# Kernel tuning notes

Hardware: AMD Instinct MI355X
Metric: run time of the kernel (lower is better)

## Reference

```python
import jax, jax.numpy as jnp
import numpy as np

IN_DIM = 1024
OUT_DIM = 1024
L = 4
HIDDEN = 64
EMB_DIM = 2 + 2 * 2 * L  # 18
BATCH = 8192
W0 = 30.0


def make_embedded_coords():
    gy, gx = jnp.meshgrid(jnp.linspace(-1.0, 1.0, OUT_DIM), jnp.linspace(-1.0, 1.0, IN_DIM), indexing='ij')
    coords = jnp.stack([gy, gx], axis=-1).reshape(-1, 2)  # [rows*cols, 2]
    embeds = [coords]
    for i in range(L):
        freq = 2.0 ** i
        embeds.append(jnp.sin(freq * jnp.pi * coords))
        embeds.append(jnp.cos(freq * jnp.pi * coords))
    return jnp.concatenate(embeds, axis=-1)  # [rows*cols, 18]


def setup_inputs() -> dict:
    key = jax.random.key(0)
    ks = jax.random.split(key, 8)
    # init scales matching torch code
    u = lambda k, shape, b: jax.random.uniform(k, shape, jnp.float32, -b, b)
    W1 = u(ks[0], (HIDDEN, EMB_DIM), 1.0 / EMB_DIM)
    b1 = u(ks[1], (HIDDEN,), 1.0 / np.sqrt(EMB_DIM))
    s2 = np.sqrt(6.0 / HIDDEN) / W0
    W2 = u(ks[2], (HIDDEN, HIDDEN), s2)
    b2 = u(ks[3], (HIDDEN,), 1.0 / np.sqrt(HIDDEN))
    W3 = u(ks[4], (1, HIDDEN), s2)
    b3 = u(ks[5], (1,), 1.0 / np.sqrt(HIDDEN))
    x = jax.random.normal(ks[6], (BATCH, IN_DIM), jnp.float32)
    bias = jnp.zeros((OUT_DIM,), jnp.float32)
    return {
        'x': x,
        'embedded_coords': make_embedded_coords(),
        'W1': W1, 'b1': b1, 'W2': W2, 'b2': b2, 'W3': W3, 'b3': b3,
        'bias': bias,
    }


def reference(x, embedded_coords, W1, b1, W2, b2, W3, b3, bias):
    rows = bias.shape[0]
    cols = x.shape[-1]
    # tiny fully-fused hypernet MLP over rows*cols coordinate points
    h = jnp.sin(W0 * (embedded_coords @ W1.T + b1))  # [rows*cols, 64]
    h = jnp.sin(W0 * (h @ W2.T + b2))                # [rows*cols, 64]
    W = (h @ W3.T + b3).reshape(rows, cols)          # generated weight
    return x @ W.T + bias                            # [batch, out_dim]
```

## Files before the change

### kernel.cpp

```cpp
#include <hip/hip_runtime.h>
#include <hip/hip_bf16.h>


typedef __attribute__((ext_vector_type(8))) short bf16x8;
typedef __attribute__((ext_vector_type(4))) float f32x4;

#define SIN_SCALE 4.77464829275686f

__device__ __forceinline__ unsigned short f2bf(float f) {
    union { float f; unsigned u; } v; v.f = f;
    unsigned r = v.u + 0x7fffu + ((v.u >> 16) & 1u);
    return (unsigned short)(r >> 16);
}

__device__ __forceinline__ unsigned pktrunc(float a, float b) {
    union { float f; unsigned u; } x, y; x.f = a; y.f = b;
    return (x.u >> 16) | (y.u & 0xffff0000u);
}

__device__ __forceinline__ float sinrev(float x) {
    return __builtin_amdgcn_sinf(x);
}

template <int OFF>
__device__ __forceinline__ float swz_add(float v) {
    return v + __int_as_float(__builtin_amdgcn_ds_swizzle(__float_as_int(v), OFF));
}

__device__ __forceinline__ void async_ld16(const void* g, void* l) {
    __builtin_amdgcn_global_load_lds(
        (__attribute__((address_space(1))) void*)g,
        (__attribute__((address_space(3))) void*)l, 16, 0, 0);
}

__global__ __launch_bounds__(256) void prep_kernel(
        const float4* __restrict__ x, unsigned short* __restrict__ xb,
        const float* __restrict__ ec,
        const float* __restrict__ W1, const float* __restrict__ b1,
        float* __restrict__ Zrow, float* __restrict__ Zcol) {
    int b = blockIdx.x;
    if (b < 8192) {
        long i = (long)b * 256 + threadIdx.x;
        float4 v = x[i];
        ushort4 o;
        o.x = f2bf(v.x); o.y = f2bf(v.y); o.z = f2bf(v.z); o.w = f2bf(v.w);
        *(ushort4*)(xb + i * 4) = o;
    } else {
        int idx = (b - 8192) * 256 + threadIdx.x;
        int j = idx & 63;
        int t = idx >> 6;
        const float* wr = W1 + j * 18;
        if (t < 1024) {
            const float* pe = ec + (long)t * 1024 * 18;
            float z = b1[j];
            #pragma unroll
            for (int i = 0; i < 18; ++i) z += wr[i] * pe[i];
            Zrow[t * 64 + j] = SIN_SCALE * z;
        } else {
            int c = t - 1024;
            const float* pe = ec + (long)c * 18;
            float z = 0.f;
            #pragma unroll
            for (int i = 0; i < 18; ++i) z += wr[i] * (pe[i] - ec[i]);
            Zcol[c * 64 + j] = SIN_SCALE * z;
        }
    }
}

__global__ __launch_bounds__(256, 3) void siren_w_kernel(
        const float* __restrict__ Zrow, const float* __restrict__ Zcol,
        const float* __restrict__ W2, const float* __restrict__ b2,
        const float* __restrict__ W3, const float* __restrict__ b3,
        unsigned short* __restrict__ Wout) {
    int lane = threadIdx.x & 63;
    int wv   = threadIdx.x >> 6;
    int ln   = lane & 15;
    int kq   = lane >> 4;

    bf16x8 bfrag[2][4];
    #pragma unroll
    for (int kc = 0; kc < 2; ++kc)
        #pragma unroll
        for (int nt = 0; nt < 4; ++nt) {
            const float* src = W2 + (nt * 16 + ln) * 64 + kc * 32 + kq * 8;
            union { bf16x8 v; unsigned u[4]; } tmp;
            #pragma unroll
            for (int q = 0; q < 4; ++q)
                tmp.u[q] = pktrunc(SIN_SCALE * src[2*q], SIN_SCALE * src[2*q + 1]);
            bfrag[kc][nt] = tmp.v;
        }
    float b2v[4], w3v[4];
    #pragma unroll
    for (int nt = 0; nt < 4; ++nt) {
        b2v[nt] = SIN_SCALE * b2[nt * 16 + ln];
        w3v[nt] = W3[nt * 16 + ln];
    }
    float b3s = b3[0];

    int wid = blockIdx.x * 4 + wv;
    int r   = wid >> 2;
    int c0  = (wid & 3) * 256;

    const float* zrp = Zrow + (long)r * 64 + kq * 8;
    float zr0[8], zr1[8];
    #pragma unroll
    for (int j = 0; j < 8; ++j) { zr0[j] = zrp[j]; zr1[j] = zrp[32 + j]; }

    for (int it = 0; it < 8; ++it) {
        int ca = c0 + it * 32 + ln;
        const float* zca = Zcol + (long)ca * 64 + kq * 8;
        const float* zcb = zca + 16 * 64;

        float sa0[8], sa1[8], sb0[8], sb1[8];
        #pragma unroll
        for (int j = 0; j < 8; ++j) {
            sa0[j] = sinrev(zr0[j] + zca[j]);
            sa1[j] = sinrev(zr1[j] + zca[32 + j]);
            sb0[j] = sinrev(zr0[j] + zcb[j]);
            sb1[j] = sinrev(zr1[j] + zcb[32 + j]);
        }
        union { bf16x8 v; unsigned u[4]; } a0, a1, bb0, bb1;
        #pragma unroll
        for (int q = 0; q < 4; ++q) {
            a0.u[q]  = pktrunc(sa0[2*q], sa0[2*q + 1]);
            a1.u[q]  = pktrunc(sa1[2*q], sa1[2*q + 1]);
            bb0.u[q] = pktrunc(sb0[2*q], sb0[2*q + 1]);
            bb1.u[q] = pktrunc(sb1[2*q], sb1[2*q + 1]);
        }

        f32x4 acca[4] = {}, accb[4] = {};
        #pragma unroll
        for (int nt = 0; nt < 4; ++nt) {
            acca[nt] = __builtin_amdgcn_mfma_f32_16x16x32_bf16(a0.v,  bfrag[0][nt], acca[nt], 0, 0, 0);
            accb[nt] = __builtin_amdgcn_mfma_f32_16x16x32_bf16(bb0.v, bfrag[0][nt], accb[nt], 0, 0, 0);
            acca[nt] = __builtin_amdgcn_mfma_f32_16x16x32_bf16(a1.v,  bfrag[1][nt], acca[nt], 0, 0, 0);
            accb[nt] = __builtin_amdgcn_mfma_f32_16x16x32_bf16(bb1.v, bfrag[1][nt], accb[nt], 0, 0, 0);
        }

        float pa[4], pb[4];
        #pragma unroll
        for (int rg = 0; rg < 4; ++rg) {
            float s = 0.f, t2 = 0.f;
            #pragma unroll
            for (int nt = 0; nt < 4; ++nt) {
                s  += w3v[nt] * sinrev(acca[nt][rg] + b2v[nt]);
                t2 += w3v[nt] * sinrev(accb[nt][rg] + b2v[nt]);
            }
            pa[rg] = s; pb[rg] = t2;
        }
        #pragma unroll
        for (int rg = 0; rg < 4; ++rg) {
            pa[rg] = swz_add<0x041F>(pa[rg]);  pb[rg] = swz_add<0x041F>(pb[rg]);
            pa[rg] = swz_add<0x081F>(pa[rg]);  pb[rg] = swz_add<0x081F>(pb[rg]);
            pa[rg] = swz_add<0x101F>(pa[rg]);  pb[rg] = swz_add<0x101F>(pb[rg]);
            pa[rg] = swz_add<0x201F>(pa[rg]);  pb[rg] = swz_add<0x201F>(pb[rg]);
        }

        if (ln == 0) {
            long p0 = (long)r * 1024 + c0 + it * 32;
            ushort4 oa, ob;
            oa.x = f2bf(pa[0] + b3s); oa.y = f2bf(pa[1] + b3s);
            oa.z = f2bf(pa[2] + b3s); oa.w = f2bf(pa[3] + b3s);
            ob.x = f2bf(pb[0] + b3s); ob.y = f2bf(pb[1] + b3s);
            ob.z = f2bf(pb[2] + b3s); ob.w = f2bf(pb[3] + b3s);
            *(ushort4*)(Wout + p0 + kq * 4)      = oa;
            *(ushort4*)(Wout + p0 + 16 + kq * 4) = ob;
        }
    }
}

__global__ __launch_bounds__(256) void gemm_kernel(
        const unsigned short* __restrict__ A,
        const unsigned short* __restrict__ B,
        const float* __restrict__ bias,
        float* __restrict__ C) {
    const int K = 1024;
    __shared__ __align__(16) unsigned short As[128 * 64];
    __shared__ __align__(16) unsigned short Bs[128 * 64];

    int tid  = threadIdx.x;
    int lane = tid & 63;
    int wv   = tid >> 6;
    int wm   = wv & 1, wn = wv >> 1;
    long Abase = (long)blockIdx.x * 128 * K;
    long Bbase = (long)blockIdx.y * 128 * K;

    int sr8 = tid >> 3;
    int sl  = tid & 7;
    int rsel = lane & 15;
    int kq   = lane >> 4;

    f32x4 acc[4][4] = {};

    for (int kt = 0; kt < K; kt += 64) {
        #pragma unroll
        for (int q = 0; q < 4; ++q) {
            int row = q * 32 + sr8;
            int cc  = sl ^ (row & 7);
            const unsigned short* ga = A + Abase + (long)row * K + kt + cc * 8;
            const unsigned short* gb = B + Bbase + (long)row * K + kt + cc * 8;
            unsigned short* la = &As[(q * 256 + wv * 64) * 8];
            unsigned short* lb = &Bs[(q * 256 + wv * 64) * 8];
            async_ld16(ga, la);
            async_ld16(gb, lb);
        }
        __syncthreads();

        #pragma unroll
        for (int h = 0; h < 2; ++h) {
            bf16x8 af[4], bf[4];
            #pragma unroll
            for (int mi = 0; mi < 4; ++mi) {
                int row = wm * 64 + mi * 16 + rsel;
                int ch  = (h * 4 + kq) ^ (row & 7);
                af[mi] = *(const bf16x8*)&As[row * 64 + ch * 8];
            }
            #pragma unroll
            for (int ni = 0; ni < 4; ++ni) {
                int row = wn * 64 + ni * 16 + rsel;
                int ch  = (h * 4 + kq) ^ (row & 7);
                bf[ni] = *(const bf16x8*)&Bs[row * 64 + ch * 8];
            }
            #pragma unroll
            for (int mi = 0; mi < 4; ++mi)
                #pragma unroll
                for (int ni = 0; ni < 4; ++ni)
                    acc[mi][ni] = __builtin_amdgcn_mfma_f32_16x16x32_bf16(
                        af[mi], bf[ni], acc[mi][ni], 0, 0, 0);
        }
        __syncthreads();
    }

    int row0 = blockIdx.x * 128 + wm * 64;
    int col0 = blockIdx.y * 128 + wn * 64;
    #pragma unroll
    for (int ni = 0; ni < 4; ++ni) {
        int col = col0 + ni * 16 + rsel;
        float bv = bias[col];
        #pragma unroll
        for (int mi = 0; mi < 4; ++mi) {
            int rbase = row0 + mi * 16 + kq * 4;
            #pragma unroll
            for (int r = 0; r < 4; ++r)
                C[(long)(rbase + r) * 1024 + col] = acc[mi][ni][r] + bv;
        }
    }
}

extern "C" void kernel_launch(void* const* d_in, const int* in_sizes, int n_in,
                              void* d_out, int out_size, void* d_ws, size_t ws_size,
                              hipStream_t stream) {
    const float* x    = (const float*)d_in[0];
    const float* ec   = (const float*)d_in[1];
    const float* W1   = (const float*)d_in[2];
    const float* b1   = (const float*)d_in[3];
    const float* W2   = (const float*)d_in[4];
    const float* b2   = (const float*)d_in[5];
    const float* W3   = (const float*)d_in[6];
    const float* b3   = (const float*)d_in[7];
    const float* bias = (const float*)d_in[8];
    float* out = (float*)d_out;

    unsigned short* xb = (unsigned short*)d_ws;
    unsigned short* Wb = xb + (size_t)8192 * 1024;
    float* Zrow = (float*)(Wb + (size_t)1024 * 1024);
    float* Zcol = Zrow + 1024 * 64;

    prep_kernel<<<8704, 256, 0, stream>>>((const float4*)x, xb, ec, W1, b1, Zrow, Zcol);
    siren_w_kernel<<<1024, 256, 0, stream>>>(Zrow, Zcol, W2, b2, W3, b3, Wb);
    dim3 g(64, 8);
    gemm_kernel<<<g, 256, 0, stream>>>(xb, Wb, bias, out);
}
```

Measured before the change: 206.7 us.

## Fuse x cast into SIREN kernel and double-buffer GEMM LDS tiles

The fp32-to-bf16 cast of x moves out of the table-prep kernel into the SIREN weight-generation kernel. One SIREN block is interleaved with every eight cast blocks, so memory-bound casting can overlap the sin-heavy MFMA work, and the Z table computation becomes its own small kernel. The GEMM now uses two LDS buffers and issues async global-to-LDS loads for the next K tile before computing the current one, removing one barrier per iteration. The trade-off is that GEMM LDS use doubles to 64KB, which may reduce occupancy, and the cast blocks inherit the SIREN kernel's register-heavy launch bounds.

```diff
diff --git a/kernel.cpp b/kernel.cpp
--- a/kernel.cpp
+++ b/kernel.cpp
@@ -33,45 +33,48 @@
         (__attribute__((address_space(3))) void*)l, 16, 0, 0);
 }
 
-__global__ __launch_bounds__(256) void prep_kernel(
-        const float4* __restrict__ x, unsigned short* __restrict__ xb,
+__global__ __launch_bounds__(256) void tables_kernel(
         const float* __restrict__ ec,
         const float* __restrict__ W1, const float* __restrict__ b1,
         float* __restrict__ Zrow, float* __restrict__ Zcol) {
-    int b = blockIdx.x;
-    if (b < 8192) {
-        long i = (long)b * 256 + threadIdx.x;
+    int idx = blockIdx.x * 256 + threadIdx.x;
+    int j = idx & 63;
+    int t = idx >> 6;
+    const float* wr = W1 + j * 18;
+    if (t < 1024) {
+        const float* pe = ec + (long)t * 1024 * 18;
+        float z = b1[j];
+        #pragma unroll
+        for (int i = 0; i < 18; ++i) z += wr[i] * pe[i];
+        Zrow[t * 64 + j] = SIN_SCALE * z;
+    } else {
+        int c = t - 1024;
+        const float* pe = ec + (long)c * 18;
+        float z = 0.f;
+        #pragma unroll
+        for (int i = 0; i < 18; ++i) z += wr[i] * (pe[i] - ec[i]);
+        Zcol[c * 64 + j] = SIN_SCALE * z;
+    }
+}
+
+__global__ __launch_bounds__(256, 3) void fused_cast_siren(
+        const float4* __restrict__ x, unsigned short* __restrict__ xb,
+        const float* __restrict__ Zrow, const float* __restrict__ Zcol,
+        const float* __restrict__ W2, const float* __restrict__ b2,
+        const float* __restrict__ W3, const float* __restrict__ b3,
+        unsigned short* __restrict__ Wout) {
+    int bid = blockIdx.x;
+    int sb  = bid / 9;
+    if (bid - sb * 9 != 0) {
+        int cb = bid - sb - 1;
+        long i = (long)cb * 256 + threadIdx.x;
         float4 v = x[i];
         ushort4 o;
         o.x = f2bf(v.x); o.y = f2bf(v.y); o.z = f2bf(v.z); o.w = f2bf(v.w);
         *(ushort4*)(xb + i * 4) = o;
-    } else {
-        int idx = (b - 8192) * 256 + threadIdx.x;
-        int j = idx & 63;
-        int t = idx >> 6;
-        const float* wr = W1 + j * 18;
-        if (t < 1024) {
-            const float* pe = ec + (long)t * 1024 * 18;
-            float z = b1[j];
-            #pragma unroll
-            for (int i = 0; i < 18; ++i) z += wr[i] * pe[i];
-            Zrow[t * 64 + j] = SIN_SCALE * z;
-        } else {
-            int c = t - 1024;
-            const float* pe = ec + (long)c * 18;
-            float z = 0.f;
-            #pragma unroll
-            for (int i = 0; i < 18; ++i) z += wr[i] * (pe[i] - ec[i]);
-            Zcol[c * 64 + j] = SIN_SCALE * z;
-        }
-    }
-}
-
-__global__ __launch_bounds__(256, 3) void siren_w_kernel(
-        const float* __restrict__ Zrow, const float* __restrict__ Zcol,
-        const float* __restrict__ W2, const float* __restrict__ b2,
-        const float* __restrict__ W3, const float* __restrict__ b3,
-        unsigned short* __restrict__ Wout) {
+        return;
+    }
+
     int lane = threadIdx.x & 63;
     int wv   = threadIdx.x >> 6;
     int ln   = lane & 15;
@@ -97,7 +100,7 @@
     }
     float b3s = b3[0];
 
-    int wid = blockIdx.x * 4 + wv;
+    int wid = sb * 4 + wv;
     int r   = wid >> 2;
     int c0  = (wid & 3) * 256;
 
@@ -175,8 +178,8 @@
         const float* __restrict__ bias,
         float* __restrict__ C) {
     const int K = 1024;
-    __shared__ __align__(16) unsigned short As[128 * 64];
-    __shared__ __align__(16) unsigned short Bs[128 * 64];
+    __shared__ __align__(16) unsigned short As[2][128 * 64];
+    __shared__ __align__(16) unsigned short Bs[2][128 * 64];
 
     int tid  = threadIdx.x;
     int lane = tid & 63;
@@ -192,20 +195,21 @@
 
     f32x4 acc[4][4] = {};
 
-    for (int kt = 0; kt < K; kt += 64) {
+    auto stage = [&](int kt, int sbuf) {
         #pragma unroll
         for (int q = 0; q < 4; ++q) {
             int row = q * 32 + sr8;
             int cc  = sl ^ (row & 7);
             const unsigned short* ga = A + Abase + (long)row * K + kt + cc * 8;
             const unsigned short* gb = B + Bbase + (long)row * K + kt + cc * 8;
-            unsigned short* la = &As[(q * 256 + wv * 64) * 8];
-            unsigned short* lb = &Bs[(q * 256 + wv * 64) * 8];
+            unsigned short* la = &As[sbuf][(q * 256 + wv * 64) * 8];
+            unsigned short* lb = &Bs[sbuf][(q * 256 + wv * 64) * 8];
             async_ld16(ga, la);
             async_ld16(gb, lb);
         }
-        __syncthreads();
-
+    };
+
+    auto compute = [&](int sbuf) {
         #pragma unroll
         for (int h = 0; h < 2; ++h) {
             bf16x8 af[4], bf[4];
@@ -213,13 +217,13 @@
             for (int mi = 0; mi < 4; ++mi) {
                 int row = wm * 64 + mi * 16 + rsel;
                 int ch  = (h * 4 + kq) ^ (row & 7);
-                af[mi] = *(const bf16x8*)&As[row * 64 + ch * 8];
+                af[mi] = *(const bf16x8*)&As[sbuf][row * 64 + ch * 8];
             }
             #pragma unroll
             for (int ni = 0; ni < 4; ++ni) {
                 int row = wn * 64 + ni * 16 + rsel;
                 int ch  = (h * 4 + kq) ^ (row & 7);
-                bf[ni] = *(const bf16x8*)&Bs[row * 64 + ch * 8];
+                bf[ni] = *(const bf16x8*)&Bs[sbuf][row * 64 + ch * 8];
             }
             #pragma unroll
             for (int mi = 0; mi < 4; ++mi)
@@ -228,8 +232,18 @@
                     acc[mi][ni] = __builtin_amdgcn_mfma_f32_16x16x32_bf16(
                         af[mi], bf[ni], acc[mi][ni], 0, 0, 0);
         }
+    };
+
+    stage(0, 0);
+    __syncthreads();
+    int buf = 0;
+    for (int kt = 64; kt < K; kt += 64) {
+        stage(kt, buf ^ 1);
+        compute(buf);
         __syncthreads();
-    }
+        buf ^= 1;
+    }
+    compute(buf);
 
     int row0 = blockIdx.x * 128 + wm * 64;
     int col0 = blockIdx.y * 128 + wn * 64;
@@ -266,8 +280,9 @@
     float* Zrow = (float*)(Wb + (size_t)1024 * 1024);
     float* Zcol = Zrow + 1024 * 64;
 
-    prep_kernel<<<8704, 256, 0, stream>>>((const float4*)x, xb, ec, W1, b1, Zrow, Zcol);
-    siren_w_kernel<<<1024, 256, 0, stream>>>(Zrow, Zcol, W2, b2, W3, b3, Wb);
+    tables_kernel<<<512, 256, 0, stream>>>(ec, W1, b1, Zrow, Zcol);
+    fused_cast_siren<<<9216, 256, 0, stream>>>((const float4*)x, xb, Zrow, Zcol,
+                                               W2, b2, W3, b3, Wb);
     dim3 g(64, 8);
     gemm_kernel<<<g, 256, 0, stream>>>(xb, Wb, bias, out);
 }
```

New measurement: 215.0 us. +4.0%, slower.
